# Optimization experiments

Hardware: AMD Instinct MI355X
Metric: run time of the kernel (lower is better)

## Reference

```python
import jax, jax.numpy as jnp
import numpy as np

HEADS = 16
DIM_HEAD = 64
SCALE = DIM_HEAD ** -0.5
EPS = 1e-5


def layer_norm(x, gamma):
    mu = jnp.mean(x, axis=-1, keepdims=True)
    var = jnp.var(x, axis=-1, keepdims=True)
    return (x - mu) * jax.lax.rsqrt(var + EPS) * gamma


def setup_inputs() -> dict:
    key = jax.random.key(0)
    ks = jax.random.split(key, 5)
    B, S, D = 2, 2048, 1024
    x = jax.random.normal(ks[0], (B, S, D), dtype=jnp.float32)
    gamma = jnp.ones((D,), dtype=jnp.float32)
    Wq = jax.random.normal(ks[1], (D, HEADS * DIM_HEAD), dtype=jnp.float32) * (D ** -0.5)
    Wkv = jax.random.normal(ks[2], (D, 2 * DIM_HEAD), dtype=jnp.float32) * (D ** -0.5)
    Wo = jax.random.normal(ks[3], (HEADS * DIM_HEAD, D), dtype=jnp.float32) * ((HEADS * DIM_HEAD) ** -0.5)
    return {"x": x, "gamma": gamma, "Wq": Wq, "Wkv": Wkv, "Wo": Wo}


def reference(x, gamma, Wq, Wkv, Wo):
    B, S, D = x.shape
    kv_input = x  # context=None -> self attention
    xn = layer_norm(x, gamma)
    q = xn @ Wq                          # [B,S,H*Dh]
    kv = kv_input @ Wkv                  # [B,S,2*Dh]
    k, v = jnp.split(kv, 2, axis=-1)     # each [B,S,Dh]
    q = q.reshape(B, S, HEADS, DIM_HEAD).transpose(0, 2, 1, 3) * SCALE  # [B,H,S,Dh]
    sim = jnp.einsum('bhid,bjd->bhij', q, k)  # [B,H,S,S]
    # causal mask: triu(j - i + 1) masked
    i_idx = jnp.arange(S)[:, None]
    j_idx = jnp.arange(S)[None, :]
    neg = -jnp.finfo(sim.dtype).max
    sim = jnp.where(j_idx > i_idx, neg, sim)
    attn = jax.nn.softmax(sim, axis=-1)
    out = jnp.einsum('bhij,bjd->bhid', attn, v)  # [B,H,S,Dh]
    out = out.transpose(0, 2, 1, 3).reshape(B, S, HEADS * DIM_HEAD)
    return out @ Wo
```

## Files before the change

### kernel.cpp

```cpp
#include <hip/hip_runtime.h>

typedef unsigned short u16;
typedef __attribute__((ext_vector_type(8))) u16    u16x8;
typedef __attribute__((ext_vector_type(4))) u16    u16x4;
typedef __attribute__((ext_vector_type(2))) unsigned u32x2;
typedef __attribute__((ext_vector_type(8))) __bf16 bf16x8;
typedef __attribute__((ext_vector_type(4))) float  f32x4;
typedef __attribute__((ext_vector_type(16))) float f32x16;

__device__ __forceinline__ u16 f2bf(float f) {
    unsigned u = __float_as_uint(f);
    u += 0x7fffu + ((u >> 16) & 1u);
    return (u16)(u >> 16);
}
__device__ __forceinline__ bf16x8 ldbf8(const u16* p) {
    return __builtin_bit_cast(bf16x8, *(const u16x8*)p);
}
__device__ __forceinline__ f32x4 mfma16(bf16x8 a, bf16x8 b, f32x4 c) {
    return __builtin_amdgcn_mfma_f32_16x16x32_bf16(a, b, c, 0, 0, 0);
}
__device__ __forceinline__ f32x16 mfma32x(bf16x8 a, bf16x8 b, f32x16 c) {
    return __builtin_amdgcn_mfma_f32_32x32x16_bf16(a, b, c, 0, 0, 0);
}
__device__ __forceinline__ float exp2a(float x) {
    float r; asm("v_exp_f32 %0, %1" : "=v"(r) : "v"(x)); return r;
}
__device__ __forceinline__ unsigned cvtpk(float lo, float hiv) {
    unsigned r; asm("v_cvt_pk_bf16_f32 %0, %1, %2" : "=v"(r) : "v"(lo), "v"(hiv)); return r;
}
__device__ __forceinline__ u32x2 permswap2(unsigned a, unsigned b) {
    return __builtin_amdgcn_permlane32_swap(a, b, false, false);
}
__device__ __forceinline__ float combine_sum(float x) {
    u32x2 pr = permswap2(__float_as_uint(x), __float_as_uint(x));
    return __uint_as_float(pr[0]) + __uint_as_float(pr[1]);
}
__device__ __forceinline__ bf16x8 pack4(unsigned a, unsigned b, unsigned c, unsigned d) {
    union { unsigned u[4]; bf16x8 v; } t; t.u[0] = a; t.u[1] = b; t.u[2] = c; t.u[3] = d; return t.v;
}

__global__ __launch_bounds__(256) void prep_kernel(const float* __restrict__ x, const float* __restrict__ gamma,
                                                   const float* __restrict__ Wq, const float* __restrict__ Wkv,
                                                   const float* __restrict__ Wo, u16* __restrict__ xn,
                                                   u16* __restrict__ xb, u16* __restrict__ Wq_t,
                                                   u16* __restrict__ Wkv_t, u16* __restrict__ Wo_t, float qscale) {
    const int bid = blockIdx.x, tid = threadIdx.x;
    if (bid < 4096) {
        const int row = bid;
        const float4 v = ((const float4*)(x + (size_t)row * 1024))[tid];
        float s  = v.x + v.y + v.z + v.w;
        float s2 = v.x * v.x + v.y * v.y + v.z * v.z + v.w * v.w;
#pragma unroll
        for (int off = 32; off; off >>= 1) { s += __shfl_down(s, off); s2 += __shfl_down(s2, off); }
        __shared__ float red[2][4];
        const int w = tid >> 6, lane = tid & 63;
        if (lane == 0) { red[0][w] = s; red[1][w] = s2; }
        __syncthreads();
        s  = red[0][0] + red[0][1] + red[0][2] + red[0][3];
        s2 = red[1][0] + red[1][1] + red[1][2] + red[1][3];
        const float mu  = s * (1.0f / 1024.0f);
        const float var = s2 * (1.0f / 1024.0f) - mu * mu;
        const float rs  = rsqrtf(var + 1e-5f);
        const float4 g = ((const float4*)gamma)[tid];
        u16x4 on, ob;
        on.x = f2bf((v.x - mu) * rs * g.x); on.y = f2bf((v.y - mu) * rs * g.y);
        on.z = f2bf((v.z - mu) * rs * g.z); on.w = f2bf((v.w - mu) * rs * g.w);
        ob.x = f2bf(v.x); ob.y = f2bf(v.y); ob.z = f2bf(v.z); ob.w = f2bf(v.w);
        ((u16x4*)(xn + (size_t)row * 1024))[tid] = on;
        ((u16x4*)(xb + (size_t)row * 1024))[tid] = ob;
    } else {
        __shared__ float tile[32][33];
        int bt = bid - 4096;
        int by = bt >> 5;
        const float* W; u16* Wt; int N; float scale;
        if (by < 32)      { W = Wq;  Wt = Wq_t;  N = 1024; scale = qscale; }
        else if (by < 36) { W = Wkv; Wt = Wkv_t; N = 128;  by -= 32; scale = 1.0f; }
        else              { W = Wo;  Wt = Wo_t;  N = 1024; by -= 36; scale = 1.0f; }
        const int K = 1024;
        const int kb = (bt & 31) * 32, nb = by * 32;
        const int tx = tid & 31, ty = tid >> 5;
#pragma unroll
        for (int i = 0; i < 32; i += 8)
            tile[ty + i][tx] = W[(size_t)(kb + ty + i) * N + nb + tx];
        __syncthreads();
#pragma unroll
        for (int i = 0; i < 32; i += 8)
            Wt[(size_t)(nb + ty + i) * K + kb + tx] = f2bf(tile[tx][ty + i] * scale);
    }
}

template<int EPI>
__device__ __forceinline__ void gemm_core(u16* lds, float (*kred)[128],
                                          const u16* __restrict__ A, const u16* __restrict__ Bt,
                                          u16* __restrict__ Cb, float* __restrict__ Cf, u16* __restrict__ Cv,
                                          int N, int K, int bx, int by, int tid) {
    constexpr int BM = 128, BN = 64, BK = 64;
    constexpr int WM = 64, WN = 32, FM = 4, FN = 2;
    constexpr int CPR = BK / 8, MS = CPR - 1;
    constexpr int CHA = BM * CPR, CH = (BM + BN) * CPR, ITERS = CH / 256;
    constexpr int LB = (BM + BN) * BK;
    const int m0 = bx * BM, n0 = by * BN;
    const int w = tid >> 6, lane = tid & 63, cl = lane & 15, kg = lane >> 4;
    const int wr = w >> 1, wc = w & 1;

    auto stage = [&](int buf, int k0) {
#pragma unroll
        for (int it = 0; it < ITERS; ++it) {
            int c = it * 256 + tid;
            const u16* g;
            if (c < CHA) { int r = c / CPR, cc = c & MS; g = A  + (size_t)(m0 + r) * K + k0 + ((cc ^ (r & MS)) * 8); }
            else { int c2 = c - CHA; int r = c2 / CPR, cc = c2 & MS; g = Bt + (size_t)(n0 + r) * K + k0 + ((cc ^ (r & MS)) * 8); }
            __builtin_amdgcn_global_load_lds(
                (const __attribute__((address_space(1))) unsigned int*)g,
                (__attribute__((address_space(3))) unsigned int*)&lds[buf * LB + c * 8], 16, 0, 0);
        }
    };

    const f32x4 zero = {0.f, 0.f, 0.f, 0.f};
    f32x4 acc[FM][FN];
#pragma unroll
    for (int m = 0; m < FM; m++)
#pragma unroll
        for (int n = 0; n < FN; n++) acc[m][n] = zero;

    const int KT = K / BK;
    stage(0, 0);
    for (int t = 0; t < KT; ++t) {
        __syncthreads();
        if (t + 1 < KT) stage((t + 1) & 1, (t + 1) * BK);
        const u16* As = &lds[(t & 1) * LB];
        const u16* Bs = &lds[(t & 1) * LB + BM * BK];
#pragma unroll
        for (int s = 0; s < BK / 32; s++) {
            bf16x8 af[FM], bfr[FN];
#pragma unroll
            for (int m = 0; m < FM; m++) {
                const int ra = wr * WM + m * 16 + cl;
                af[m] = ldbf8(As + ra * BK + (((s * 4 + kg) ^ (ra & MS)) * 8));
            }
#pragma unroll
            for (int n = 0; n < FN; n++) {
                const int rb = wc * WN + n * 16 + cl;
                bfr[n] = ldbf8(Bs + rb * BK + (((s * 4 + kg) ^ (rb & MS)) * 8));
            }
#pragma unroll
            for (int m = 0; m < FM; m++)
#pragma unroll
                for (int n = 0; n < FN; n++) acc[m][n] = mfma16(af[m], bfr[n], acc[m][n]);
        }
    }

#pragma unroll
    for (int m = 0; m < FM; m++)
#pragma unroll
        for (int n = 0; n < FN; n++)
#pragma unroll
            for (int r = 0; r < 4; r++) {
                const int row = m0 + wr * WM + m * 16 + kg * 4 + r;
                const int col = n0 + wc * WN + n * 16 + cl;
                const float v = acc[m][n][r];
                if constexpr (EPI == 0) Cb[(size_t)row * N + col] = f2bf(v);
                else if constexpr (EPI == 1) Cf[(size_t)row * N + col] = v;
                else {
                    if (col < 64) Cb[(size_t)row * 64 + col] = f2bf(v);
                    else { int bb = row >> 11, s = row & 2047;
                           Cv[((size_t)bb * 64 + (col - 64)) * 2048 + s] = f2bf(v); }
                }
            }

    if constexpr (EPI == 2) {
        if (n0 == 0) {
            float s2[FM][4];
#pragma unroll
            for (int m = 0; m < FM; m++)
#pragma unroll
                for (int r = 0; r < 4; r++) {
                    float t = 0.f;
#pragma unroll
                    for (int n = 0; n < FN; n++) {
                        const float vb = __uint_as_float(((unsigned)f2bf(acc[m][n][r])) << 16);
                        t = fmaf(vb, vb, t);
                    }
                    s2[m][r] = t;
                }
#pragma unroll
            for (int off = 1; off < 16; off <<= 1)
#pragma unroll
                for (int m = 0; m < FM; m++)
#pragma unroll
                    for (int r = 0; r < 4; r++) s2[m][r] += __shfl_xor(s2[m][r], off);
            if (cl == 0)
#pragma unroll
                for (int m = 0; m < FM; m++)
#pragma unroll
                    for (int r = 0; r < 4; r++) kred[wc][wr * 64 + m * 16 + kg * 4 + r] = s2[m][r];
            __syncthreads();
            if (tid < 64) {
                float t = fmaxf(kred[0][tid] + kred[1][tid], kred[0][tid + 64] + kred[1][tid + 64]);
#pragma unroll
                for (int off = 1; off < 64; off <<= 1) t = fmaxf(t, __shfl_xor(t, off));
                if (tid == 0) Cf[bx] = t;
            }
        }
    }
}

__global__ __launch_bounds__(256, 2) void gemm_qkv(const u16* __restrict__ xn, const u16* __restrict__ Wq_t,
                                                   u16* __restrict__ qb, const u16* __restrict__ xb,
                                                   const u16* __restrict__ Wkv_t, u16* __restrict__ kb,
                                                   u16* __restrict__ vtb, float* __restrict__ kpart) {
    __shared__ __align__(16) u16 lds[2 * 192 * 64];
    __shared__ float kred[2][128];
    const int tid = threadIdx.x;
    const int nwg = gridDim.x;
    int lin = blockIdx.x;
    lin = (lin & 7) * (nwg >> 3) + (lin >> 3);
    if (lin < 512) gemm_core<0>(lds, kred, xn, Wq_t, qb, nullptr, nullptr, 1024, 1024, lin & 31, lin >> 5, tid);
    else { int l2 = lin - 512; gemm_core<2>(lds, kred, xb, Wkv_t, kb, kpart, vtb, 128, 1024, l2 & 31, l2 >> 5, tid); }
}

__global__ __launch_bounds__(256, 2) void gemm_o(const u16* __restrict__ attb, const u16* __restrict__ Wo_t,
                                                 float* __restrict__ out) {
    __shared__ __align__(16) u16 lds[2 * 192 * 64];
    __shared__ float kred[2][128];
    const int tid = threadIdx.x;
    const int nwg = gridDim.x;
    int lin = blockIdx.x;
    lin = (lin & 7) * (nwg >> 3) + (lin >> 3);
    gemm_core<1>(lds, kred, attb, Wo_t, nullptr, out, nullptr, 1024, 1024, lin & 31, lin >> 5, tid);
}

__global__ __launch_bounds__(256, 2) void attn_fwd(const u16* __restrict__ q, const u16* __restrict__ k,
                                                   const u16* __restrict__ vt, const float* __restrict__ kpart,
                                                   u16* __restrict__ o) {
    constexpr int S = 2048;
    const int bid = blockIdx.x;
    const int p = (bid < 256) ? (bid >> 5) : (15 - ((bid - 256) >> 5));
    const int bh = bid & 31;
    const int h = bh & 15, b = bh >> 4;
    const int tid = threadIdx.x, w = tid >> 6, lane = tid & 63;
    const int pw = w & 1, par = w >> 1;
    const int l31 = lane & 31;
    const bool hi = (lane & 32) != 0;
    const int hi1 = hi ? 1 : 0, hi8 = hi ? 8 : 0;
    const int t1 = 2 * p + pw, t2 = 63 - t1;
    const int iters = 32 - p;
    const size_t bS = (size_t)b * S;

    __shared__ __align__(16) u16 smem[18432];

    auto stageK = [&](int jt, int buf, int tl) {
        const int r = tid >> 3, c = tid & 7;
        const u16* gp = k + (bS + jt * 32 + r) * 64 + ((c ^ (r & 7)) * 8);
        __builtin_amdgcn_global_load_lds(
            (const __attribute__((address_space(1))) unsigned int*)gp,
            (__attribute__((address_space(3))) unsigned int*)(smem + (buf * 2 + tl) * 2048 + tid * 8), 16, 0, 0);
    };
    auto loadV = [&](int jt) -> u16x8 {
        const int rv = tid >> 2, c4 = tid & 3;
        return *(const u16x8*)(vt + ((size_t)b * 64 + rv) * S + jt * 32 + c4 * 8);
    };
    auto writeV = [&](int buf, int tl, u16x8 v) {
        const int rv = tid >> 2, c4 = tid & 3;
        *(u16x8*)(smem + 8192 + (buf * 2 + tl) * 2560 + rv * 40 + c4 * 8) = v;
    };

    float km = kpart[(b << 4) + (l31 & 15)];
#pragma unroll
    for (int off = 1; off < 16; off <<= 1) km = fmaxf(km, __shfl_xor(km, off));
    const float kmaxb = sqrtf(km);

    bf16x8 qf1[4], qf2[4];
    float mB1, mB2;
    auto qload = [&](int t, bf16x8 (&qf)[4]) -> float {
        const u16* qp = q + (bS + t * 32 + l31) * 1024 + h * 64 + hi8;
        float qn2 = 0.f;
#pragma unroll
        for (int sub = 0; sub < 4; sub++) {
            qf[sub] = ldbf8(qp + sub * 16);
            const u16x8 uv = __builtin_bit_cast(u16x8, qf[sub]);
#pragma unroll
            for (int j = 0; j < 8; j++) {
                const float v = __uint_as_float(((unsigned)uv[j]) << 16);
                qn2 = fmaf(v, v, qn2);
            }
        }
        return sqrtf(combine_sum(qn2)) * kmaxb;
    };
    mB1 = qload(t1, qf1);
    mB2 = qload(t2, qf2);

    f32x16 a1lo, a1hi, a2lo, a2hi;
#pragma unroll
    for (int r = 0; r < 16; r++) { a1lo[r] = 0.f; a1hi[r] = 0.f; a2lo[r] = 0.f; a2hi[r] = 0.f; }
    float l1 = 0.f, l2 = 0.f;

    auto process = [&](const bf16x8 (&qf)[4], const bf16x8 (&kf)[4],
                       const bf16x8& vf00, const bf16x8& vf01, const bf16x8& vf10, const bf16x8& vf11,
                       f32x16& a0, f32x16& a1, float& lr, float mB, bool diag) {
        f32x16 s;
#pragma unroll
        for (int r = 0; r < 16; r++) s[r] = -mB;
#pragma unroll
        for (int sub = 0; sub < 4; sub++) s = mfma32x(kf[sub], qf[sub], s);
        if (diag) {
#pragma unroll
            for (int r = 0; r < 16; r++) {
                const int kvl = (r & 3) + 8 * (r >> 2) + (hi ? 4 : 0);
                if (kvl > l31) s[r] = -1e30f;
            }
        }
        float p0 = 0.f, p1 = 0.f;
#pragma unroll
        for (int r = 0; r < 16; r += 2) {
            const float ea = exp2a(s[r]);
            const float eb = exp2a(s[r + 1]);
            s[r] = ea; s[r + 1] = eb;
            p0 += ea; p1 += eb;
        }
        lr += p0 + p1;
        unsigned w0 = cvtpk(s[0], s[1]),  w1 = cvtpk(s[2], s[3]);
        unsigned w2 = cvtpk(s[4], s[5]),  w3 = cvtpk(s[6], s[7]);
        u32x2 r02 = permswap2(w0, w2), r13 = permswap2(w1, w3);
        bf16x8 pf0 = pack4(r02[0], r13[0], r02[1], r13[1]);
        unsigned y0 = cvtpk(s[8], s[9]),   y1 = cvtpk(s[10], s[11]);
        unsigned y2 = cvtpk(s[12], s[13]), y3 = cvtpk(s[14], s[15]);
        u32x2 t02 = permswap2(y0, y2), t13 = permswap2(y1, y3);
        bf16x8 pf1 = pack4(t02[0], t13[0], t02[1], t13[1]);
        a0 = mfma32x(vf00, pf0, a0);
        a0 = mfma32x(vf01, pf1, a0);
        a1 = mfma32x(vf10, pf0, a1);
        a1 = mfma32x(vf11, pf1, a1);
    };

    stageK(0, 0, 0); stageK(1, 0, 1);
    u16x8 v0 = loadV(0), v1 = loadV(1);
    for (int i = 0; i < iters; i++) {
        const int buf = i & 1;
        writeV(buf, 0, v0); writeV(buf, 1, v1);
        __syncthreads();
        if (i + 1 < iters) {
            stageK(2 * i + 2, buf ^ 1, 0); stageK(2 * i + 3, buf ^ 1, 1);
            v0 = loadV(2 * i + 2); v1 = loadV(2 * i + 3);
        }
        const int jt = 2 * i + par;
        if (jt <= t2) {
            const u16* kcur = smem + (buf * 2 + par) * 2048;
            const u16* vcur = smem + 8192 + (buf * 2 + par) * 2560;
            bf16x8 kf[4];
#pragma unroll
            for (int sub = 0; sub < 4; sub++)
                kf[sub] = ldbf8(kcur + l31 * 64 + (((sub * 2 + hi1) ^ (l31 & 7)) * 8));
            const bf16x8 vf00 = ldbf8(vcur + l31 * 40 + hi8);
            const bf16x8 vf01 = ldbf8(vcur + l31 * 40 + 16 + hi8);
            const bf16x8 vf10 = ldbf8(vcur + (32 + l31) * 40 + hi8);
            const bf16x8 vf11 = ldbf8(vcur + (32 + l31) * 40 + 16 + hi8);
            if (jt <= t1) process(qf1, kf, vf00, vf01, vf10, vf11, a1lo, a1hi, l1, mB1, jt == t1);
            process(qf2, kf, vf00, vf01, vf10, vf11, a2lo, a2hi, l2, mB2, jt == t2);
        }
    }
    float l1t = combine_sum(l1), l2t = combine_sum(l2);

    float* fm = (float*)smem;
    __syncthreads();
    {
        float* dst = fm + (((pw * 2) + (par ? 0 : 1)) * 64 + lane) * 36;
        if (par) { *(f32x16*)dst = a1lo; *(f32x16*)(dst + 16) = a1hi; dst[32] = l1t; }
        else     { *(f32x16*)dst = a2lo; *(f32x16*)(dst + 16) = a2hi; dst[32] = l2t; }
    }
    __syncthreads();
    {
        const float* src = fm + (((pw * 2) + (par ? 1 : 0)) * 64 + lane) * 36;
        const f32x16 s0 = *(const f32x16*)src;
        const f32x16 s1 = *(const f32x16*)(src + 16);
        if (par) {
#pragma unroll
            for (int r = 0; r < 16; r++) { a2lo[r] += s0[r]; a2hi[r] += s1[r]; }
            l2t += src[32];
        } else {
#pragma unroll
            for (int r = 0; r < 16; r++) { a1lo[r] += s0[r]; a1hi[r] += s1[r]; }
            l1t += src[32];
        }
    }
    __syncthreads();

    auto epi = [&](const f32x16& a0, const f32x16& a1, float lt, int t) {
        const float rl = 1.0f / lt;
        u16* lb = smem + w * 2304;
#pragma unroll
        for (int i = 0; i < 8; i++) {
            const int d = ((2 * i) & 3) + 8 * ((2 * i) >> 2) + (hi ? 4 : 0);
            *(unsigned*)&lb[l31 * 72 + d]      = cvtpk(a0[2 * i] * rl, a0[2 * i + 1] * rl);
            *(unsigned*)&lb[l31 * 72 + 32 + d] = cvtpk(a1[2 * i] * rl, a1[2 * i + 1] * rl);
        }
        asm volatile("s_waitcnt lgkmcnt(0)" ::: "memory");
#pragma unroll
        for (int i = 0; i < 4; i++) {
            const int qq = i * 8 + (lane >> 3), dd = (lane & 7) * 8;
            *(u16x8*)(o + (bS + t * 32 + qq) * 1024 + h * 64 + dd) = *(const u16x8*)&lb[qq * 72 + dd];
        }
    };
    if (par == 0) epi(a1lo, a1hi, l1t, t1);
    else          epi(a2lo, a2hi, l2t, t2);
}

extern "C" void kernel_launch(void* const* d_in, const int* in_sizes, int n_in,
                              void* d_out, int out_size, void* d_ws, size_t ws_size,
                              hipStream_t stream) {
    const float* x     = (const float*)d_in[0];
    const float* gamma = (const float*)d_in[1];
    const float* Wq    = (const float*)d_in[2];
    const float* Wkv   = (const float*)d_in[3];
    const float* Wo    = (const float*)d_in[4];
    float* out = (float*)d_out;
    char* ws = (char*)d_ws;

    u16* Wq_t  = (u16*)(ws + 0);
    u16* Wo_t  = (u16*)(ws + (2u << 20));
    u16* Wkv_t = (u16*)(ws + (4u << 20));
    u16* xn    = (u16*)(ws + 4456448u);
    u16* xb    = (u16*)(ws + 12845056u);
    u16* qb    = (u16*)(ws + 21233664u);
    u16* kb    = (u16*)(ws + 29622272u);
    u16* vtb   = (u16*)(ws + 30146560u);
    u16* attb  = (u16*)(ws + 30670848u);
    float* kpart = (float*)(ws + 39059456u);

    const float qscale = 0.125f * 1.44269504f;
    prep_kernel<<<4096 + 2176, 256, 0, stream>>>(x, gamma, Wq, Wkv, Wo, xn, xb, Wq_t, Wkv_t, Wo_t, qscale);
    gemm_qkv<<<576, 256, 0, stream>>>(xn, Wq_t, qb, xb, Wkv_t, kb, vtb, kpart);
    attn_fwd<<<512, 256, 0, stream>>>(qb, kb, vtb, kpart, attb);
    gemm_o<<<512, 256, 0, stream>>>(attb, Wo_t, out);
}
```

Measured before the change: 79.47 us.

## Deepen K/V prefetch pipeline to four LDS stages with explicit vmcnt waits

Replaces the double-buffered K/V staging loop in the attention kernel with a four-slot ring buffer, prefetching three iterations ahead. V loads are issued through inline asm global_load_dwordx4, and the loop waits with manual s_waitcnt vmcnt counts and a raw s_barrier instead of __syncthreads. The aim is to hide more global memory latency behind the MFMA work. In exchange, LDS use doubles to 72KB per block, which may cut the two-blocks-per-CU occupancy, and the hand-written wait counts are fragile if the compiler adds other outstanding loads.

```diff
diff --git a/kernel.cpp b/kernel.cpp
--- a/kernel.cpp
+++ b/kernel.cpp
@@ -4,6 +4,7 @@
 typedef __attribute__((ext_vector_type(8))) u16    u16x8;
 typedef __attribute__((ext_vector_type(4))) u16    u16x4;
 typedef __attribute__((ext_vector_type(2))) unsigned u32x2;
+typedef __attribute__((ext_vector_type(4))) unsigned u32x4;
 typedef __attribute__((ext_vector_type(8))) __bf16 bf16x8;
 typedef __attribute__((ext_vector_type(4))) float  f32x4;
 typedef __attribute__((ext_vector_type(16))) float f32x16;
@@ -247,22 +248,25 @@
     const int iters = 32 - p;
     const size_t bS = (size_t)b * S;
 
-    __shared__ __align__(16) u16 smem[18432];
-
-    auto stageK = [&](int jt, int buf, int tl) {
+    __shared__ __align__(16) u16 smem[36864];
+
+    auto stageK = [&](int jt, int set, int tl) {
         const int r = tid >> 3, c = tid & 7;
         const u16* gp = k + (bS + jt * 32 + r) * 64 + ((c ^ (r & 7)) * 8);
         __builtin_amdgcn_global_load_lds(
             (const __attribute__((address_space(1))) unsigned int*)gp,
-            (__attribute__((address_space(3))) unsigned int*)(smem + (buf * 2 + tl) * 2048 + tid * 8), 16, 0, 0);
-    };
-    auto loadV = [&](int jt) -> u16x8 {
+            (__attribute__((address_space(3))) unsigned int*)(smem + set * 9216 + tl * 2048 + tid * 8), 16, 0, 0);
+    };
+    auto loadVa = [&](int jt) -> u16x8 {
         const int rv = tid >> 2, c4 = tid & 3;
-        return *(const u16x8*)(vt + ((size_t)b * 64 + rv) * S + jt * 32 + c4 * 8);
-    };
-    auto writeV = [&](int buf, int tl, u16x8 v) {
+        const u16* ap = vt + ((size_t)b * 64 + rv) * S + jt * 32 + c4 * 8;
+        u32x4 d;
+        asm volatile("global_load_dwordx4 %0, %1, off" : "=v"(d) : "v"(ap) : "memory");
+        return __builtin_bit_cast(u16x8, d);
+    };
+    auto writeV = [&](int set, int tl, u16x8 v) {
         const int rv = tid >> 2, c4 = tid & 3;
-        *(u16x8*)(smem + 8192 + (buf * 2 + tl) * 2560 + rv * 40 + c4 * 8) = v;
+        *(u16x8*)(smem + set * 9216 + 4096 + tl * 2560 + rv * 40 + c4 * 8) = v;
     };
 
     float km = kpart[(b << 4) + (l31 & 15)];
@@ -333,32 +337,50 @@
         a1 = mfma32x(vf11, pf1, a1);
     };
 
-    stageK(0, 0, 0); stageK(1, 0, 1);
-    u16x8 v0 = loadV(0), v1 = loadV(1);
-    for (int i = 0; i < iters; i++) {
-        const int buf = i & 1;
-        writeV(buf, 0, v0); writeV(buf, 1, v1);
-        __syncthreads();
-        if (i + 1 < iters) {
-            stageK(2 * i + 2, buf ^ 1, 0); stageK(2 * i + 3, buf ^ 1, 1);
-            v0 = loadV(2 * i + 2); v1 = loadV(2 * i + 3);
-        }
-        const int jt = 2 * i + par;
-        if (jt <= t2) {
-            const u16* kcur = smem + (buf * 2 + par) * 2048;
-            const u16* vcur = smem + 8192 + (buf * 2 + par) * 2560;
-            bf16x8 kf[4];
-#pragma unroll
-            for (int sub = 0; sub < 4; sub++)
-                kf[sub] = ldbf8(kcur + l31 * 64 + (((sub * 2 + hi1) ^ (l31 & 7)) * 8));
-            const bf16x8 vf00 = ldbf8(vcur + l31 * 40 + hi8);
-            const bf16x8 vf01 = ldbf8(vcur + l31 * 40 + 16 + hi8);
-            const bf16x8 vf10 = ldbf8(vcur + (32 + l31) * 40 + hi8);
-            const bf16x8 vf11 = ldbf8(vcur + (32 + l31) * 40 + 16 + hi8);
-            if (jt <= t1) process(qf1, kf, vf00, vf01, vf10, vf11, a1lo, a1hi, l1, mB1, jt == t1);
-            process(qf2, kf, vf00, vf01, vf10, vf11, a2lo, a2hi, l2, mB2, jt == t2);
-        }
-    }
+    u16x8 va0, vb0, va1, vb1, va2, vb2, va3, vb3;
+    stageK(0, 0, 0); stageK(1, 0, 1); va0 = loadVa(0); vb0 = loadVa(1);
+    stageK(2, 1, 0); stageK(3, 1, 1); va1 = loadVa(2); vb1 = loadVa(3);
+    stageK(4, 2, 0); stageK(5, 2, 1); va2 = loadVa(4); vb2 = loadVa(5);
+
+#define ABODY(I, SLOT, vaC, vbC, vaN, vbN)                                          \
+    if ((I) < iters) {                                                              \
+        if ((I) + 2 < iters)      asm volatile("s_waitcnt vmcnt(8)" ::: "memory");  \
+        else if ((I) + 1 < iters) asm volatile("s_waitcnt vmcnt(4)" ::: "memory");  \
+        else                      asm volatile("s_waitcnt vmcnt(0)" ::: "memory");  \
+        writeV(SLOT, 0, vaC); writeV(SLOT, 1, vbC);                                 \
+        asm volatile("s_waitcnt lgkmcnt(0)" ::: "memory");                          \
+        __builtin_amdgcn_s_barrier();                                               \
+        __builtin_amdgcn_sched_barrier(0);                                          \
+        if ((I) + 3 < iters) {                                                      \
+            stageK(2 * ((I) + 3),     ((SLOT) + 3) & 3, 0);                         \
+            stageK(2 * ((I) + 3) + 1, ((SLOT) + 3) & 3, 1);                         \
+            vaN = loadVa(2 * ((I) + 3)); vbN = loadVa(2 * ((I) + 3) + 1);           \
+        }                                                                           \
+        const int jt = 2 * (I) + par;                                               \
+        if (jt <= t2) {                                                             \
+            const u16* kcur = smem + (SLOT) * 9216 + par * 2048;                    \
+            const u16* vcur = smem + (SLOT) * 9216 + 4096 + par * 2560;             \
+            bf16x8 kf[4];                                                           \
+            _Pragma("unroll")                                                       \
+            for (int sub = 0; sub < 4; sub++)                                       \
+                kf[sub] = ldbf8(kcur + l31 * 64 + (((sub * 2 + hi1) ^ (l31 & 7)) * 8)); \
+            const bf16x8 vf00 = ldbf8(vcur + l31 * 40 + hi8);                       \
+            const bf16x8 vf01 = ldbf8(vcur + l31 * 40 + 16 + hi8);                  \
+            const bf16x8 vf10 = ldbf8(vcur + (32 + l31) * 40 + hi8);                \
+            const bf16x8 vf11 = ldbf8(vcur + (32 + l31) * 40 + 16 + hi8);           \
+            if (jt <= t1) process(qf1, kf, vf00, vf01, vf10, vf11, a1lo, a1hi, l1, mB1, jt == t1); \
+            process(qf2, kf, vf00, vf01, vf10, vf11, a2lo, a2hi, l2, mB2, jt == t2); \
+        }                                                                           \
+    }
+
+    for (int ii = 0; ii < 32; ii += 4) {
+        ABODY(ii + 0, 0, va0, vb0, va3, vb3)
+        ABODY(ii + 1, 1, va1, vb1, va0, vb0)
+        ABODY(ii + 2, 2, va2, vb2, va1, vb1)
+        ABODY(ii + 3, 3, va3, vb3, va2, vb2)
+    }
+#undef ABODY
+    asm volatile("s_waitcnt vmcnt(0)" ::: "memory");
     float l1t = combine_sum(l1), l2t = combine_sum(l2);
 
     float* fm = (float*)smem;
```

Measured after the change: 79.35 us. About the same (-0.1%).

## Double attention workgroup to 512 threads with four-way KV split and tree reduction

Applied to the files above, without the earlier changes.

Launches the attention kernel with 8 waves per workgroup. Each iteration stages four K/V tiles into a larger double-buffered LDS area, so four wave-pairs each process a different KV tile. Partial accumulators and row sums are merged with a two-level LDS tree reduction before the first two waves write the output. This adds parallelism within each block at the cost of more LDS, extra reduction passes, and a tight launch bound, __launch_bounds__(512, 4), that may force register spilling.

```diff
diff --git a/kernel.cpp b/kernel.cpp
--- a/kernel.cpp
+++ b/kernel.cpp
@@ -230,7 +230,7 @@
     gemm_core<1>(lds, kred, attb, Wo_t, nullptr, out, nullptr, 1024, 1024, lin & 31, lin >> 5, tid);
 }
 
-__global__ __launch_bounds__(256, 2) void attn_fwd(const u16* __restrict__ q, const u16* __restrict__ k,
+__global__ __launch_bounds__(512, 4) void attn_fwd(const u16* __restrict__ q, const u16* __restrict__ k,
                                                    const u16* __restrict__ vt, const float* __restrict__ kpart,
                                                    u16* __restrict__ o) {
     constexpr int S = 2048;
@@ -244,25 +244,48 @@
     const bool hi = (lane & 32) != 0;
     const int hi1 = hi ? 1 : 0, hi8 = hi ? 8 : 0;
     const int t1 = 2 * p + pw, t2 = 63 - t1;
-    const int iters = 32 - p;
+    const int kvmax = 63 - 2 * p;
+    const int iters = (64 - 2 * p + 3) >> 2;
     const size_t bS = (size_t)b * S;
 
-    __shared__ __align__(16) u16 smem[18432];
-
-    auto stageK = [&](int jt, int buf, int tl) {
-        const int r = tid >> 3, c = tid & 7;
-        const u16* gp = k + (bS + jt * 32 + r) * 64 + ((c ^ (r & 7)) * 8);
-        __builtin_amdgcn_global_load_lds(
-            (const __attribute__((address_space(1))) unsigned int*)gp,
-            (__attribute__((address_space(3))) unsigned int*)(smem + (buf * 2 + tl) * 2048 + tid * 8), 16, 0, 0);
-    };
-    auto loadV = [&](int jt) -> u16x8 {
-        const int rv = tid >> 2, c4 = tid & 3;
-        return *(const u16x8*)(vt + ((size_t)b * 64 + rv) * S + jt * 32 + c4 * 8);
-    };
-    auto writeV = [&](int buf, int tl, u16x8 v) {
-        const int rv = tid >> 2, c4 = tid & 3;
-        *(u16x8*)(smem + 8192 + (buf * 2 + tl) * 2560 + rv * 40 + c4 * 8) = v;
+    __shared__ __align__(16) u16 smem[36864];
+
+    auto stageK4 = [&](int i, int buf) {
+#pragma unroll
+        for (int it = 0; it < 2; ++it) {
+            const int c = it * 512 + tid;
+            const int tile = c >> 8, cc = c & 255;
+            const int jt = 4 * i + tile;
+            if (jt <= kvmax) {
+                const int r = cc >> 3, ch = cc & 7;
+                const u16* gp = k + (bS + jt * 32 + r) * 64 + ((ch ^ (r & 7)) * 8);
+                __builtin_amdgcn_global_load_lds(
+                    (const __attribute__((address_space(1))) unsigned int*)gp,
+                    (__attribute__((address_space(3))) unsigned int*)(smem + buf * 18432 + tile * 2048 + cc * 8),
+                    16, 0, 0);
+            }
+        }
+    };
+    auto loadV4 = [&](int i, u16x8 (&vr)[2]) {
+#pragma unroll
+        for (int it = 0; it < 2; ++it) {
+            const int c = it * 512 + tid;
+            const int tile = c >> 8, cc = c & 255;
+            const int jt = 4 * i + tile;
+            if (jt <= kvmax) {
+                const int row = cc >> 2, ch = cc & 3;
+                vr[it] = *(const u16x8*)(vt + ((size_t)b * 64 + row) * S + jt * 32 + ch * 8);
+            }
+        }
+    };
+    auto writeV4 = [&](int buf, const u16x8 (&vr)[2]) {
+#pragma unroll
+        for (int it = 0; it < 2; ++it) {
+            const int c = it * 512 + tid;
+            const int tile = c >> 8, cc = c & 255;
+            const int row = cc >> 2, ch = cc & 3;
+            *(u16x8*)(smem + buf * 18432 + 8192 + tile * 2560 + row * 40 + ch * 8) = vr[it];
+        }
     };
 
     float km = kpart[(b << 4) + (l31 & 15)];
@@ -333,20 +356,18 @@
         a1 = mfma32x(vf11, pf1, a1);
     };
 
-    stageK(0, 0, 0); stageK(1, 0, 1);
-    u16x8 v0 = loadV(0), v1 = loadV(1);
+    u16x8 vr[2];
+    stageK4(0, 0);
+    loadV4(0, vr);
     for (int i = 0; i < iters; i++) {
         const int buf = i & 1;
-        writeV(buf, 0, v0); writeV(buf, 1, v1);
+        writeV4(buf, vr);
         __syncthreads();
-        if (i + 1 < iters) {
-            stageK(2 * i + 2, buf ^ 1, 0); stageK(2 * i + 3, buf ^ 1, 1);
-            v0 = loadV(2 * i + 2); v1 = loadV(2 * i + 3);
-        }
-        const int jt = 2 * i + par;
+        if (i + 1 < iters) { stageK4(i + 1, buf ^ 1); loadV4(i + 1, vr); }
+        const int jt = 4 * i + par;
         if (jt <= t2) {
-            const u16* kcur = smem + (buf * 2 + par) * 2048;
-            const u16* vcur = smem + 8192 + (buf * 2 + par) * 2560;
+            const u16* kcur = smem + buf * 18432 + par * 2048;
+            const u16* vcur = smem + buf * 18432 + 8192 + par * 2560;
             bf16x8 kf[4];
 #pragma unroll
             for (int sub = 0; sub < 4; sub++)
@@ -362,47 +383,49 @@
     float l1t = combine_sum(l1), l2t = combine_sum(l2);
 
     float* fm = (float*)smem;
+    auto dump = [&](int slot) {
+        float* d = fm + ((size_t)slot * 64 + lane) * 68;
+        *(f32x16*)d        = a1lo; *(f32x16*)(d + 16) = a1hi;
+        *(f32x16*)(d + 32) = a2lo; *(f32x16*)(d + 48) = a2hi;
+        d[64] = l1t; d[65] = l2t;
+    };
+    auto absorb = [&](int slot) {
+        const float* sp = fm + ((size_t)slot * 64 + lane) * 68;
+        const f32x16 b0 = *(const f32x16*)sp,        b1 = *(const f32x16*)(sp + 16);
+        const f32x16 b2 = *(const f32x16*)(sp + 32), b3 = *(const f32x16*)(sp + 48);
+#pragma unroll
+        for (int r = 0; r < 16; r++) { a1lo[r] += b0[r]; a1hi[r] += b1[r]; a2lo[r] += b2[r]; a2hi[r] += b3[r]; }
+        l1t += sp[64]; l2t += sp[65];
+    };
     __syncthreads();
-    {
-        float* dst = fm + (((pw * 2) + (par ? 0 : 1)) * 64 + lane) * 36;
-        if (par) { *(f32x16*)dst = a1lo; *(f32x16*)(dst + 16) = a1hi; dst[32] = l1t; }
-        else     { *(f32x16*)dst = a2lo; *(f32x16*)(dst + 16) = a2hi; dst[32] = l2t; }
+    if (w >= 4) dump(w - 4);
+    __syncthreads();
+    if (w < 4) absorb(w);
+    __syncthreads();
+    if (w == 2 || w == 3) dump(w - 2);
+    __syncthreads();
+    if (w < 2) absorb(w);
+    __syncthreads();
+    if (w < 2) {
+        auto epi = [&](const f32x16& a0, const f32x16& a1, float lt, int t, int which) {
+            const float rl = 1.0f / lt;
+            u16* lb = smem + (w * 2 + which) * 2304;
+#pragma unroll
+            for (int i = 0; i < 8; i++) {
+                const int d = ((2 * i) & 3) + 8 * ((2 * i) >> 2) + (hi ? 4 : 0);
+                *(unsigned*)&lb[l31 * 72 + d]      = cvtpk(a0[2 * i] * rl, a0[2 * i + 1] * rl);
+                *(unsigned*)&lb[l31 * 72 + 32 + d] = cvtpk(a1[2 * i] * rl, a1[2 * i + 1] * rl);
+            }
+            asm volatile("s_waitcnt lgkmcnt(0)" ::: "memory");
+#pragma unroll
+            for (int i = 0; i < 4; i++) {
+                const int qq = i * 8 + (lane >> 3), dd = (lane & 7) * 8;
+                *(u16x8*)(o + (bS + t * 32 + qq) * 1024 + h * 64 + dd) = *(const u16x8*)&lb[qq * 72 + dd];
+            }
+        };
+        epi(a1lo, a1hi, l1t, t1, 0);
+        epi(a2lo, a2hi, l2t, t2, 1);
     }
-    __syncthreads();
-    {
-        const float* src = fm + (((pw * 2) + (par ? 1 : 0)) * 64 + lane) * 36;
-        const f32x16 s0 = *(const f32x16*)src;
-        const f32x16 s1 = *(const f32x16*)(src + 16);
-        if (par) {
-#pragma unroll
-            for (int r = 0; r < 16; r++) { a2lo[r] += s0[r]; a2hi[r] += s1[r]; }
-            l2t += src[32];
-        } else {
-#pragma unroll
-            for (int r = 0; r < 16; r++) { a1lo[r] += s0[r]; a1hi[r] += s1[r]; }
-            l1t += src[32];
-        }
-    }
-    __syncthreads();
-
-    auto epi = [&](const f32x16& a0, const f32x16& a1, float lt, int t) {
-        const float rl = 1.0f / lt;
-        u16* lb = smem + w * 2304;
-#pragma unroll
-        for (int i = 0; i < 8; i++) {
-            const int d = ((2 * i) & 3) + 8 * ((2 * i) >> 2) + (hi ? 4 : 0);
-            *(unsigned*)&lb[l31 * 72 + d]      = cvtpk(a0[2 * i] * rl, a0[2 * i + 1] * rl);
-            *(unsigned*)&lb[l31 * 72 + 32 + d] = cvtpk(a1[2 * i] * rl, a1[2 * i + 1] * rl);
-        }
-        asm volatile("s_waitcnt lgkmcnt(0)" ::: "memory");
-#pragma unroll
-        for (int i = 0; i < 4; i++) {
-            const int qq = i * 8 + (lane >> 3), dd = (lane & 7) * 8;
-            *(u16x8*)(o + (bS + t * 32 + qq) * 1024 + h * 64 + dd) = *(const u16x8*)&lb[qq * 72 + dd];
-        }
-    };
-    if (par == 0) epi(a1lo, a1hi, l1t, t1);
-    else          epi(a2lo, a2hi, l2t, t2);
 }
 
 extern "C" void kernel_launch(void* const* d_in, const int* in_sizes, int n_in,
@@ -430,6 +453,6 @@
     const float qscale = 0.125f * 1.44269504f;
     prep_kernel<<<4096 + 2176, 256, 0, stream>>>(x, gamma, Wq, Wkv, Wo, xn, xb, Wq_t, Wkv_t, Wo_t, qscale);
     gemm_qkv<<<576, 256, 0, stream>>>(xn, Wq_t, qb, xb, Wkv_t, kb, vtb, kpart);
-    attn_fwd<<<512, 256, 0, stream>>>(qb, kb, vtb, kpart, attb);
+    attn_fwd<<<512, 512, 0, stream>>>(qb, kb, vtb, kpart, attb);
     gemm_o<<<512, 256, 0, stream>>>(attb, Wo_t, out);
 }
```

New measurement: 286.7 us. 261% more time.

## Split attention work across 8 waves, one query tile per wave pair

Applied to the files above, without the earlier changes.

The attention kernel moves from 256 to 512 threads per block. Each pair of waves now owns a single query tile instead of each wave processing two query tiles, which halves per-wave accumulator registers and doubles the number of waves sharing each staged K/V tile. K and V staging is spread across all 512 threads, and the cross-parity reduction plus epilogue are rewritten for the new wave mapping. Wave-level parallelism should rise and register pressure fall, but each K/V fragment loaded from LDS is reused by one query tile per wave instead of two, so more LDS reads are needed. Higher launch bounds also constrain registers.

```diff
diff --git a/kernel.cpp b/kernel.cpp
--- a/kernel.cpp
+++ b/kernel.cpp
@@ -230,7 +230,7 @@
     gemm_core<1>(lds, kred, attb, Wo_t, nullptr, out, nullptr, 1024, 1024, lin & 31, lin >> 5, tid);
 }
 
-__global__ __launch_bounds__(256, 2) void attn_fwd(const u16* __restrict__ q, const u16* __restrict__ k,
+__global__ __launch_bounds__(512, 4) void attn_fwd(const u16* __restrict__ q, const u16* __restrict__ k,
                                                    const u16* __restrict__ vt, const float* __restrict__ kpart,
                                                    u16* __restrict__ o) {
     constexpr int S = 2048;
@@ -239,30 +239,33 @@
     const int bh = bid & 31;
     const int h = bh & 15, b = bh >> 4;
     const int tid = threadIdx.x, w = tid >> 6, lane = tid & 63;
-    const int pw = w & 1, par = w >> 1;
+    const int ti = w >> 1, par = w & 1;
     const int l31 = lane & 31;
     const bool hi = (lane & 32) != 0;
     const int hi1 = hi ? 1 : 0, hi8 = hi ? 8 : 0;
-    const int t1 = 2 * p + pw, t2 = 63 - t1;
+    const int tw = (ti < 2) ? (2 * p + ti) : ((ti == 2) ? 62 - 2 * p : 63 - 2 * p);
     const int iters = 32 - p;
     const size_t bS = (size_t)b * S;
 
     __shared__ __align__(16) u16 smem[18432];
 
-    auto stageK = [&](int jt, int buf, int tl) {
-        const int r = tid >> 3, c = tid & 7;
-        const u16* gp = k + (bS + jt * 32 + r) * 64 + ((c ^ (r & 7)) * 8);
+    auto stageK2 = [&](int i, int buf) {
+        const int tile = tid >> 8, cc = tid & 255;
+        const int r = cc >> 3, ch = cc & 7;
+        const u16* gp = k + (bS + (2 * i + tile) * 32 + r) * 64 + ((ch ^ (r & 7)) * 8);
         __builtin_amdgcn_global_load_lds(
             (const __attribute__((address_space(1))) unsigned int*)gp,
-            (__attribute__((address_space(3))) unsigned int*)(smem + (buf * 2 + tl) * 2048 + tid * 8), 16, 0, 0);
+            (__attribute__((address_space(3))) unsigned int*)(smem + (buf * 2 + tile) * 2048 + cc * 8), 16, 0, 0);
     };
-    auto loadV = [&](int jt) -> u16x8 {
-        const int rv = tid >> 2, c4 = tid & 3;
-        return *(const u16x8*)(vt + ((size_t)b * 64 + rv) * S + jt * 32 + c4 * 8);
+    auto loadV2 = [&](int i) -> u16x8 {
+        const int tile = tid >> 8, cc = tid & 255;
+        const int row = cc >> 2, ch = cc & 3;
+        return *(const u16x8*)(vt + ((size_t)b * 64 + row) * S + (2 * i + tile) * 32 + ch * 8);
     };
-    auto writeV = [&](int buf, int tl, u16x8 v) {
-        const int rv = tid >> 2, c4 = tid & 3;
-        *(u16x8*)(smem + 8192 + (buf * 2 + tl) * 2560 + rv * 40 + c4 * 8) = v;
+    auto writeV2 = [&](int buf, u16x8 v) {
+        const int tile = tid >> 8, cc = tid & 255;
+        const int row = cc >> 2, ch = cc & 3;
+        *(u16x8*)(smem + 8192 + (buf * 2 + tile) * 2560 + row * 40 + ch * 8) = v;
     };
 
     float km = kpart[(b << 4) + (l31 & 15)];
@@ -270,10 +273,10 @@
     for (int off = 1; off < 16; off <<= 1) km = fmaxf(km, __shfl_xor(km, off));
     const float kmaxb = sqrtf(km);
 
-    bf16x8 qf1[4], qf2[4];
-    float mB1, mB2;
-    auto qload = [&](int t, bf16x8 (&qf)[4]) -> float {
-        const u16* qp = q + (bS + t * 32 + l31) * 1024 + h * 64 + hi8;
+    bf16x8 qf[4];
+    float mB;
+    {
+        const u16* qp = q + (bS + tw * 32 + l31) * 1024 + h * 64 + hi8;
         float qn2 = 0.f;
 #pragma unroll
         for (int sub = 0; sub < 4; sub++) {
@@ -285,66 +288,24 @@
                 qn2 = fmaf(v, v, qn2);
             }
         }
-        return sqrtf(combine_sum(qn2)) * kmaxb;
-    };
-    mB1 = qload(t1, qf1);
-    mB2 = qload(t2, qf2);
-
-    f32x16 a1lo, a1hi, a2lo, a2hi;
-#pragma unroll
-    for (int r = 0; r < 16; r++) { a1lo[r] = 0.f; a1hi[r] = 0.f; a2lo[r] = 0.f; a2hi[r] = 0.f; }
-    float l1 = 0.f, l2 = 0.f;
-
-    auto process = [&](const bf16x8 (&qf)[4], const bf16x8 (&kf)[4],
-                       const bf16x8& vf00, const bf16x8& vf01, const bf16x8& vf10, const bf16x8& vf11,
-                       f32x16& a0, f32x16& a1, float& lr, float mB, bool diag) {
-        f32x16 s;
-#pragma unroll
-        for (int r = 0; r < 16; r++) s[r] = -mB;
-#pragma unroll
-        for (int sub = 0; sub < 4; sub++) s = mfma32x(kf[sub], qf[sub], s);
-        if (diag) {
-#pragma unroll
-            for (int r = 0; r < 16; r++) {
-                const int kvl = (r & 3) + 8 * (r >> 2) + (hi ? 4 : 0);
-                if (kvl > l31) s[r] = -1e30f;
-            }
-        }
-        float p0 = 0.f, p1 = 0.f;
-#pragma unroll
-        for (int r = 0; r < 16; r += 2) {
-            const float ea = exp2a(s[r]);
-            const float eb = exp2a(s[r + 1]);
-            s[r] = ea; s[r + 1] = eb;
-            p0 += ea; p1 += eb;
-        }
-        lr += p0 + p1;
-        unsigned w0 = cvtpk(s[0], s[1]),  w1 = cvtpk(s[2], s[3]);
-        unsigned w2 = cvtpk(s[4], s[5]),  w3 = cvtpk(s[6], s[7]);
-        u32x2 r02 = permswap2(w0, w2), r13 = permswap2(w1, w3);
-        bf16x8 pf0 = pack4(r02[0], r13[0], r02[1], r13[1]);
-        unsigned y0 = cvtpk(s[8], s[9]),   y1 = cvtpk(s[10], s[11]);
-        unsigned y2 = cvtpk(s[12], s[13]), y3 = cvtpk(s[14], s[15]);
-        u32x2 t02 = permswap2(y0, y2), t13 = permswap2(y1, y3);
-        bf16x8 pf1 = pack4(t02[0], t13[0], t02[1], t13[1]);
-        a0 = mfma32x(vf00, pf0, a0);
-        a0 = mfma32x(vf01, pf1, a0);
-        a1 = mfma32x(vf10, pf0, a1);
-        a1 = mfma32x(vf11, pf1, a1);
-    };
-
-    stageK(0, 0, 0); stageK(1, 0, 1);
-    u16x8 v0 = loadV(0), v1 = loadV(1);
+        mB = sqrtf(combine_sum(qn2)) * kmaxb;
+    }
+
+    f32x16 a0, a1;
+#pragma unroll
+    for (int r = 0; r < 16; r++) { a0[r] = 0.f; a1[r] = 0.f; }
+    float l = 0.f;
+
+    u16x8 vr;
+    stageK2(0, 0);
+    vr = loadV2(0);
     for (int i = 0; i < iters; i++) {
         const int buf = i & 1;
-        writeV(buf, 0, v0); writeV(buf, 1, v1);
+        writeV2(buf, vr);
         __syncthreads();
-        if (i + 1 < iters) {
-            stageK(2 * i + 2, buf ^ 1, 0); stageK(2 * i + 3, buf ^ 1, 1);
-            v0 = loadV(2 * i + 2); v1 = loadV(2 * i + 3);
-        }
+        if (i + 1 < iters) { stageK2(i + 1, buf ^ 1); vr = loadV2(i + 1); }
         const int jt = 2 * i + par;
-        if (jt <= t2) {
+        if (jt <= tw) {
             const u16* kcur = smem + (buf * 2 + par) * 2048;
             const u16* vcur = smem + 8192 + (buf * 2 + par) * 2560;
             bf16x8 kf[4];
@@ -355,39 +316,63 @@
             const bf16x8 vf01 = ldbf8(vcur + l31 * 40 + 16 + hi8);
             const bf16x8 vf10 = ldbf8(vcur + (32 + l31) * 40 + hi8);
             const bf16x8 vf11 = ldbf8(vcur + (32 + l31) * 40 + 16 + hi8);
-            if (jt <= t1) process(qf1, kf, vf00, vf01, vf10, vf11, a1lo, a1hi, l1, mB1, jt == t1);
-            process(qf2, kf, vf00, vf01, vf10, vf11, a2lo, a2hi, l2, mB2, jt == t2);
-        }
-    }
-    float l1t = combine_sum(l1), l2t = combine_sum(l2);
+            f32x16 s;
+#pragma unroll
+            for (int r = 0; r < 16; r++) s[r] = -mB;
+#pragma unroll
+            for (int sub = 0; sub < 4; sub++) s = mfma32x(kf[sub], qf[sub], s);
+            if (jt == tw) {
+#pragma unroll
+                for (int r = 0; r < 16; r++) {
+                    const int kvl = (r & 3) + 8 * (r >> 2) + (hi ? 4 : 0);
+                    if (kvl > l31) s[r] = -1e30f;
+                }
+            }
+            float p0 = 0.f, p1 = 0.f;
+#pragma unroll
+            for (int r = 0; r < 16; r += 2) {
+                const float ea = exp2a(s[r]);
+                const float eb = exp2a(s[r + 1]);
+                s[r] = ea; s[r + 1] = eb;
+                p0 += ea; p1 += eb;
+            }
+            l += p0 + p1;
+            unsigned w0 = cvtpk(s[0], s[1]),  w1 = cvtpk(s[2], s[3]);
+            unsigned w2 = cvtpk(s[4], s[5]),  w3 = cvtpk(s[6], s[7]);
+            u32x2 r02 = permswap2(w0, w2), r13 = permswap2(w1, w3);
+            bf16x8 pf0 = pack4(r02[0], r13[0], r02[1], r13[1]);
+            unsigned y0 = cvtpk(s[8], s[9]),   y1 = cvtpk(s[10], s[11]);
+            unsigned y2 = cvtpk(s[12], s[13]), y3 = cvtpk(s[14], s[15]);
+            u32x2 t02 = permswap2(y0, y2), t13 = permswap2(y1, y3);
+            bf16x8 pf1 = pack4(t02[0], t13[0], t02[1], t13[1]);
+            a0 = mfma32x(vf00, pf0, a0);
+            a0 = mfma32x(vf01, pf1, a0);
+            a1 = mfma32x(vf10, pf0, a1);
+            a1 = mfma32x(vf11, pf1, a1);
+        }
+    }
+    float lt = combine_sum(l);
 
     float* fm = (float*)smem;
     __syncthreads();
-    {
-        float* dst = fm + (((pw * 2) + (par ? 0 : 1)) * 64 + lane) * 36;
-        if (par) { *(f32x16*)dst = a1lo; *(f32x16*)(dst + 16) = a1hi; dst[32] = l1t; }
-        else     { *(f32x16*)dst = a2lo; *(f32x16*)(dst + 16) = a2hi; dst[32] = l2t; }
+    if (par == 1) {
+        float* d = fm + ((size_t)(ti * 64) + lane) * 36;
+        *(f32x16*)d        = a0;
+        *(f32x16*)(d + 16) = a1;
+        d[32] = lt;
     }
     __syncthreads();
-    {
-        const float* src = fm + (((pw * 2) + (par ? 1 : 0)) * 64 + lane) * 36;
-        const f32x16 s0 = *(const f32x16*)src;
-        const f32x16 s1 = *(const f32x16*)(src + 16);
-        if (par) {
-#pragma unroll
-            for (int r = 0; r < 16; r++) { a2lo[r] += s0[r]; a2hi[r] += s1[r]; }
-            l2t += src[32];
-        } else {
-#pragma unroll
-            for (int r = 0; r < 16; r++) { a1lo[r] += s0[r]; a1hi[r] += s1[r]; }
-            l1t += src[32];
-        }
+    if (par == 0) {
+        const float* sp = fm + ((size_t)(ti * 64) + lane) * 36;
+        const f32x16 b0 = *(const f32x16*)sp, b1 = *(const f32x16*)(sp + 16);
+#pragma unroll
+        for (int r = 0; r < 16; r++) { a0[r] += b0[r]; a1[r] += b1[r]; }
+        lt += sp[32];
     }
     __syncthreads();
-
-    auto epi = [&](const f32x16& a0, const f32x16& a1, float lt, int t) {
+    if (par == 0) {
         const float rl = 1.0f / lt;
-        u16* lb = smem + w * 2304;
+        u16* lb = smem + ti * 2304;
 #pragma unroll
         for (int i = 0; i < 8; i++) {
             const int d = ((2 * i) & 3) + 8 * ((2 * i) >> 2) + (hi ? 4 : 0);
@@ -398,11 +383,9 @@
 #pragma unroll
         for (int i = 0; i < 4; i++) {
             const int qq = i * 8 + (lane >> 3), dd = (lane & 7) * 8;
-            *(u16x8*)(o + (bS + t * 32 + qq) * 1024 + h * 64 + dd) = *(const u16x8*)&lb[qq * 72 + dd];
-        }
-    };
-    if (par == 0) epi(a1lo, a1hi, l1t, t1);
-    else          epi(a2lo, a2hi, l2t, t2);
+            *(u16x8*)(o + (bS + tw * 32 + qq) * 1024 + h * 64 + dd) = *(const u16x8*)&lb[qq * 72 + dd];
+        }
+    }
 }
 
 extern "C" void kernel_launch(void* const* d_in, const int* in_sizes, int n_in,
@@ -430,6 +413,6 @@
     const float qscale = 0.125f * 1.44269504f;
     prep_kernel<<<4096 + 2176, 256, 0, stream>>>(x, gamma, Wq, Wkv, Wo, xn, xb, Wq_t, Wkv_t, Wo_t, qscale);
     gemm_qkv<<<576, 256, 0, stream>>>(xn, Wq_t, qb, xb, Wkv_t, kb, vtb, kpart);
-    attn_fwd<<<512, 256, 0, stream>>>(qb, kb, vtb, kpart, attb);
+    attn_fwd<<<512, 512, 0, stream>>>(qb, kb, vtb, kpart, attb);
     gemm_o<<<512, 256, 0, stream>>>(attb, Wo_t, out);
 }
```

New measurement: 80.54 us. Within noise of the previous version (+1.4%).
